# Optimization experiments

Measured on AMD Instinct MI355X. Metric: run time of the kernel, lower is better.

Reference implementation:

```python
import jax, jax.numpy as jnp
import numpy as np

C_Z = 128
C_H = 128
EPS = 1e-5


def _layer_norm(x, g, b):
    mu = jnp.mean(x, axis=-1, keepdims=True)
    var = jnp.var(x, axis=-1, keepdims=True)
    return (x - mu) * jax.lax.rsqrt(var + EPS) * g + b


def setup_inputs() -> dict:
    key = jax.random.key(0)
    ks = jax.random.split(key, 8)
    B, N = 1, 512
    z = jax.random.normal(ks[0], (B, N, N, C_Z), dtype=jnp.float32)
    mask = jnp.ones((B, N, N), dtype=jnp.float32)
    s = 0.02
    return {
        "z": z,
        "mask": mask,
        "ln_in_g": jnp.ones((C_Z,), jnp.float32),
        "ln_in_b": jnp.zeros((C_Z,), jnp.float32),
        "w_ap": jax.random.normal(ks[1], (C_Z, C_H), jnp.float32) * s,
        "b_ap": jnp.zeros((C_H,), jnp.float32),
        "w_ag": jax.random.normal(ks[2], (C_Z, C_H), jnp.float32) * s,
        "b_ag": jnp.zeros((C_H,), jnp.float32),
        "w_bp": jax.random.normal(ks[3], (C_Z, C_H), jnp.float32) * s,
        "b_bp": jnp.zeros((C_H,), jnp.float32),
        "w_bg": jax.random.normal(ks[4], (C_Z, C_H), jnp.float32) * s,
        "b_bg": jnp.zeros((C_H,), jnp.float32),
        "w_g": jax.random.normal(ks[5], (C_Z, C_Z), jnp.float32) * s,
        "b_g": jnp.zeros((C_Z,), jnp.float32),
        "ln_out_g": jnp.ones((C_H,), jnp.float32),
        "ln_out_b": jnp.zeros((C_H,), jnp.float32),
        "w_z": jax.random.normal(ks[6], (C_H, C_Z), jnp.float32) * s,
        "b_z": jnp.zeros((C_Z,), jnp.float32),
    }


def reference(z, mask, ln_in_g, ln_in_b, w_ap, b_ap, w_ag, b_ag,
              w_bp, b_bp, w_bg, b_bg, w_g, b_g, ln_out_g, ln_out_b, w_z, b_z):
    m = mask[..., None]                                  # [B,N,N,1]
    zn = _layer_norm(z, ln_in_g, ln_in_b)                # [B,N,N,Cz]
    a = m * jax.nn.sigmoid(zn @ w_ag + b_ag) * (zn @ w_ap + b_ap)  # [B,N,N,H]
    b = m * jax.nn.sigmoid(zn @ w_bg + b_bg) * (zn @ w_bp + b_bp)  # [B,N,N,H]
    # outgoing triangle: x[i,k] = sum_j a[i,j] * b[k,j]  (per hidden channel)
    x = jnp.einsum("bijh,bkjh->bikh", a, b)
    x = _layer_norm(x, ln_out_g, ln_out_b) @ w_z + b_z   # [B,N,N,Cz]
    g = jax.nn.sigmoid(zn @ w_g + b_g)
    return x * g
```

## Files before the change

### kernel.cpp

```cpp
#include <hip/hip_runtime.h>
#include <stdint.h>

#define NPOS 262144
#define EPS_LN 1e-5f
#define ZSTRIDE 272

typedef _Float16 f16x8_t __attribute__((ext_vector_type(8)));
typedef float f32x4_t __attribute__((ext_vector_type(4)));

static __device__ __forceinline__ unsigned short f2h(float f) {
    union { _Float16 h; unsigned short u; } v;
    v.h = (_Float16)f;
    return v.u;
}
static __device__ __forceinline__ float h2f(unsigned short u) {
    union { unsigned short u; _Float16 h; } v;
    v.u = u;
    return (float)v.h;
}
static __device__ __forceinline__ float sigmoidf_(float x) {
    return 1.0f / (1.0f + __expf(-x));
}

#define GLOAD_LDS16(gp, lp) __builtin_amdgcn_global_load_lds( \
    (const __attribute__((address_space(1))) void*)(gp), \
    (__attribute__((address_space(3))) void*)(lp), 16, 0, 0)

__global__ __launch_bounds__(256)
void k_prep6(const float* w0, const float* w1, const float* w2,
             const float* w3, const float* w4, const float* w5,
             const float* lng, const float* lnog, unsigned short* wt) {
    const float* srcs[6] = {w0, w1, w2, w3, w4, w5};
    const float* src = srcs[blockIdx.x];
    const float* fold = (blockIdx.x == 4) ? lnog : lng;
    unsigned short* dst = wt + blockIdx.x * 16384;
    for (int rep = 0; rep < 64; ++rep) {
        int idx = rep * 256 + threadIdx.x;
        int h = idx >> 7, k = idx & 127;
        dst[idx] = f2h(src[k * 128 + h] * fold[k]);
    }
}

__global__ __launch_bounds__(128)
void k_const(const float* wap, const float* wag, const float* wbp,
             const float* wbg, const float* wz, const float* wg,
             const float* lng, const float* lnb,
             const float* lnog, const float* lnob, float* cc) {
    const float* Ws[6] = {wap, wag, wbp, wbg, wz, wg};
    const float* W = Ws[blockIdx.x];
    const float* gv = (blockIdx.x == 4) ? lnog : lng;
    const float* bv = (blockIdx.x == 4) ? lnob : lnb;
    int c = threadIdx.x;
    float s1 = 0.f, s2 = 0.f;
    for (int k = 0; k < 128; ++k) {
        float wv = W[k * 128 + c];
        s1 += gv[k] * wv;
        s2 += bv[k] * wv;
    }
    cc[blockIdx.x * 256 + c] = s1;
    cc[blockIdx.x * 256 + 128 + c] = s2;
}

__global__ __launch_bounds__(512, 2)
void k1e(const float* __restrict__ z, const float* __restrict__ mask,
         const unsigned short* __restrict__ wt, const float* __restrict__ cc,
         const float* __restrict__ b_ap, const float* __restrict__ b_ag,
         const float* __restrict__ b_bp, const float* __restrict__ b_bg,
         unsigned short* __restrict__ a_t, unsigned short* __restrict__ b_t,
         unsigned short* __restrict__ z16, unsigned* __restrict__ mustd)
{
    __shared__ char sZ[128 * ZSTRIDE];
    __shared__ float smu[128];
    __shared__ float srstd[128];
    const int t = threadIdx.x;
    const int lane = t & 63;
    const int w = t >> 6;
    const int g = lane >> 4;
    const int l15 = lane & 15;
    const int h = w * 16 + l15;
    const int p0 = blockIdx.x * 128;

    {
        const int pos = t >> 2, q = t & 3;
        const float* zp = z + (size_t)(p0 + pos) * 128 + q * 32;
        float s = 0.f, s2 = 0.f;
        #pragma unroll
        for (int e = 0; e < 8; ++e) {
            float4 v = *(const float4*)(zp + e * 4);
            s += v.x + v.y + v.z + v.w;
            s2 += v.x * v.x + v.y * v.y + v.z * v.z + v.w * v.w;
            uint2 st;
            st.x = f2h(v.x) | ((unsigned)f2h(v.y) << 16);
            st.y = f2h(v.z) | ((unsigned)f2h(v.w) << 16);
            *(uint2*)(sZ + pos * ZSTRIDE + (q * 32 + e * 4) * 2) = st;
            *(uint2*)(z16 + (size_t)(p0 + pos) * 128 + q * 32 + e * 4) = st;
        }
        s  += __shfl_xor(s, 1);  s  += __shfl_xor(s, 2);
        s2 += __shfl_xor(s2, 1); s2 += __shfl_xor(s2, 2);
        float mu = s * (1.0f / 128.0f);
        float var = s2 * (1.0f / 128.0f) - mu * mu;
        float rstd = rsqrtf(var + EPS_LN);
        if (q == 0) {
            smu[pos] = mu;
            srstd[pos] = rstd;
            mustd[p0 + pos] = f2h(mu) | ((unsigned)f2h(rstd) << 16);
        }
    }

    f16x8_t wapf[4], wagf[4], wbpf[4], wbgf[4];
    #pragma unroll
    for (int kk = 0; kk < 4; ++kk) {
        int off = h * 128 + kk * 32 + g * 8;
        wapf[kk] = *(const f16x8_t*)(wt + 0 * 16384 + off);
        wagf[kk] = *(const f16x8_t*)(wt + 1 * 16384 + off);
        wbpf[kk] = *(const f16x8_t*)(wt + 2 * 16384 + off);
        wbgf[kk] = *(const f16x8_t*)(wt + 3 * 16384 + off);
    }
    const float C1ap = cc[0 * 256 + h], C2ap = cc[0 * 256 + 128 + h];
    const float C1ag = cc[1 * 256 + h], C2ag = cc[1 * 256 + 128 + h];
    const float C1bp = cc[2 * 256 + h], C2bp = cc[2 * 256 + 128 + h];
    const float C1bg = cc[3 * 256 + h], C2bg = cc[3 * 256 + 128 + h];
    const float bap = b_ap[h], bag = b_ag[h];
    const float bbp = b_bp[h], bbg = b_bg[h];
    __syncthreads();

    f32x4_t zero = {0.f, 0.f, 0.f, 0.f};
    for (int rt = 0; rt < 8; ++rt) {
        f32x4_t accAP = zero, accAG = zero, accBP = zero, accBG = zero;
        #pragma unroll
        for (int kk = 0; kk < 4; ++kk) {
            f16x8_t ax = *(const f16x8_t*)(sZ + (rt * 16 + l15) * ZSTRIDE + kk * 64 + g * 16);
            accAP = __builtin_amdgcn_mfma_f32_16x16x32_f16(ax, wapf[kk], accAP, 0, 0, 0);
            accAG = __builtin_amdgcn_mfma_f32_16x16x32_f16(ax, wagf[kk], accAG, 0, 0, 0);
            accBP = __builtin_amdgcn_mfma_f32_16x16x32_f16(ax, wbpf[kk], accBP, 0, 0, 0);
            accBG = __builtin_amdgcn_mfma_f32_16x16x32_f16(ax, wbgf[kk], accBG, 0, 0, 0);
        }
        int pb = p0 + rt * 16 + g * 4;
        unsigned short pka[4], pkb[4];
        #pragma unroll
        for (int r = 0; r < 4; ++r) {
            float mu = smu[rt * 16 + g * 4 + r];
            float rstd = srstd[rt * 16 + g * 4 + r];
            float vAP = rstd * (accAP[r] - mu * C1ap) + C2ap + bap;
            float vAG = rstd * (accAG[r] - mu * C1ag) + C2ag + bag;
            float vBP = rstd * (accBP[r] - mu * C1bp) + C2bp + bbp;
            float vBG = rstd * (accBG[r] - mu * C1bg) + C2bg + bbg;
            float m = mask[pb + r];
            pka[r] = f2h(m * sigmoidf_(vAG) * vAP);
            pkb[r] = f2h(m * sigmoidf_(vBG) * vBP);
        }
        uint2 sta, stb;
        sta.x = pka[0] | ((unsigned)pka[1] << 16);
        sta.y = pka[2] | ((unsigned)pka[3] << 16);
        stb.x = pkb[0] | ((unsigned)pkb[1] << 16);
        stb.y = pkb[2] | ((unsigned)pkb[3] << 16);
        *(uint2*)(a_t + (size_t)h * NPOS + pb) = sta;
        *(uint2*)(b_t + (size_t)h * NPOS + pb) = stb;
    }
}

__global__ __launch_bounds__(256, 2)
void k2_tri(const unsigned short* __restrict__ a_t,
            const unsigned short* __restrict__ b_t,
            unsigned short* __restrict__ x_t) {
    __shared__ char sA[16384];
    __shared__ char sB[16384];
    const int t = threadIdx.x;
    const int lane = t & 63;
    const int w = t >> 6;
    const int wr = w >> 1, wc = w & 1;
    const int h = blockIdx.y;
    const int i0 = (blockIdx.x >> 2) * 128;
    const int k0 = (blockIdx.x & 3) * 128;
    const unsigned short* Abase = a_t + (size_t)h * NPOS;
    const unsigned short* Bbase = b_t + (size_t)h * NPOS;

    f32x4_t zero = {0.f, 0.f, 0.f, 0.f};
    f32x4_t acc[4][4];
    #pragma unroll
    for (int m = 0; m < 4; ++m)
        #pragma unroll
        for (int n = 0; n < 4; ++n) acc[m][n] = zero;

    for (int kt = 0; kt < 8; ++kt) {
        #pragma unroll
        for (int pass = 0; pass < 4; ++pass) {
            int ci = pass * 256 + t;
            int row = ci >> 3, ch = ci & 7;
            const unsigned short* gA = Abase + (size_t)(i0 + row) * 512 + kt * 64 + ch * 8;
            const unsigned short* gB = Bbase + (size_t)(k0 + row) * 512 + kt * 64 + ch * 8;
            GLOAD_LDS16(gA, sA + w * 1024 + pass * 4096);
            GLOAD_LDS16(gB, sB + w * 1024 + pass * 4096);
        }
        __syncthreads();
        #pragma unroll
        for (int ks = 0; ks < 2; ++ks) {
            f16x8_t af[4], bf[4];
            #pragma unroll
            for (int m = 0; m < 4; ++m) {
                int ar = wr * 64 + m * 16 + (lane & 15);
                af[m] = *(const f16x8_t*)(sA + ar * 128 + ks * 64 + (lane >> 4) * 16);
            }
            #pragma unroll
            for (int n = 0; n < 4; ++n) {
                int br = wc * 64 + n * 16 + (lane & 15);
                bf[n] = *(const f16x8_t*)(sB + br * 128 + ks * 64 + (lane >> 4) * 16);
            }
            #pragma unroll
            for (int m = 0; m < 4; ++m)
                #pragma unroll
                for (int n = 0; n < 4; ++n)
                    acc[m][n] = __builtin_amdgcn_mfma_f32_16x16x32_f16(af[m], bf[n], acc[m][n], 0, 0, 0);
        }
        __syncthreads();
    }
    #pragma unroll
    for (int m = 0; m < 4; ++m) {
        int i = i0 + wr * 64 + m * 16 + (lane >> 4) * 4;
        #pragma unroll
        for (int n = 0; n < 4; ++n) {
            int k = k0 + wc * 64 + n * 16 + (lane & 15);
            #pragma unroll
            for (int r = 0; r < 4; ++r) {
                x_t[(size_t)h * NPOS + (size_t)(i + r) * 512 + k] = f2h(acc[m][n][r]);
            }
        }
    }
}

__global__ __launch_bounds__(512, 2)
void k3d(const unsigned short* __restrict__ x_t,
         const unsigned short* __restrict__ z16,
         const unsigned* __restrict__ mustd,
         const unsigned short* __restrict__ wt, const float* __restrict__ cc,
         const float* __restrict__ b_z, const float* __restrict__ b_g,
         float* __restrict__ out)
{
    __shared__ char sX[128 * ZSTRIDE];
    __shared__ float smuX[128], srstdX[128];
    __shared__ float smuZ[128], srstdZ[128];
    const int t = threadIdx.x, lane = t & 63, w = t >> 6;
    const int g = lane >> 4;
    const int c = w * 16 + (lane & 15);
    const int p0 = blockIdx.x * 128;

    f16x8_t wzf[4], wgf[4];
    #pragma unroll
    for (int kk = 0; kk < 4; ++kk) {
        int off = c * 128 + kk * 32 + g * 8;
        wzf[kk] = *(const f16x8_t*)(wt + 4 * 16384 + off);
        wgf[kk] = *(const f16x8_t*)(wt + 5 * 16384 + off);
    }
    const float bzv = b_z[c], bgv = b_g[c];
    const float C1z = cc[4 * 256 + c], C2z = cc[4 * 256 + 128 + c];
    const float C1g = cc[5 * 256 + c], C2g = cc[5 * 256 + 128 + c];

    if (t < 128) {
        unsigned v = mustd[p0 + t];
        smuZ[t] = h2f((unsigned short)(v & 0xffffu));
        srstdZ[t] = h2f((unsigned short)(v >> 16));
    }

    {
        const int hp = lane;
        const int ps = w * 16;
        const unsigned short* x0 = x_t + (size_t)(2 * hp) * NPOS + p0 + ps;
        const unsigned short* x1 = x_t + (size_t)(2 * hp + 1) * NPOS + p0 + ps;
        uint4 a0 = *(const uint4*)(x0);
        uint4 a1 = *(const uint4*)(x0 + 8);
        uint4 b0 = *(const uint4*)(x1);
        uint4 b1 = *(const uint4*)(x1 + 8);
        unsigned aw[8] = {a0.x, a0.y, a0.z, a0.w, a1.x, a1.y, a1.z, a1.w};
        unsigned bw[8] = {b0.x, b0.y, b0.z, b0.w, b1.x, b1.y, b1.z, b1.w};
        #pragma unroll
        for (int e = 0; e < 8; ++e) {
            int p = ps + 2 * e;
            *(unsigned*)(sX + p * ZSTRIDE + hp * 4) =
                (aw[e] & 0xffffu) | ((bw[e] & 0xffffu) << 16);
            *(unsigned*)(sX + (p + 1) * ZSTRIDE + hp * 4) =
                (aw[e] >> 16) | ((bw[e] >> 16) << 16);
        }
    }
    __syncthreads();
    {
        int pos = t >> 2, q = t & 3;
        float s = 0.f, s2 = 0.f;
        #pragma unroll
        for (int e = 0; e < 8; ++e) {
            uint2 vv = *(const uint2*)(sX + pos * ZSTRIDE + (q * 32 + e * 4) * 2);
            float v0 = h2f((unsigned short)(vv.x & 0xffffu));
            float v1 = h2f((unsigned short)(vv.x >> 16));
            float v2 = h2f((unsigned short)(vv.y & 0xffffu));
            float v3 = h2f((unsigned short)(vv.y >> 16));
            s  += v0 + v1 + v2 + v3;
            s2 += v0 * v0 + v1 * v1 + v2 * v2 + v3 * v3;
        }
        s  += __shfl_xor(s, 1);  s  += __shfl_xor(s, 2);
        s2 += __shfl_xor(s2, 1); s2 += __shfl_xor(s2, 2);
        float mu = s * (1.0f / 128.0f);
        float var = s2 * (1.0f / 128.0f) - mu * mu;
        if (q == 0) {
            smuX[pos] = mu;
            srstdX[pos] = rsqrtf(var + EPS_LN);
        }
    }
    __syncthreads();
    f32x4_t zero = {0.f, 0.f, 0.f, 0.f};
    for (int rt = 0; rt < 8; ++rt) {
        f32x4_t accX = zero, accG = zero;
        #pragma unroll
        for (int kk = 0; kk < 4; ++kk) {
            int row = rt * 16 + (lane & 15);
            f16x8_t ax = *(const f16x8_t*)(sX + row * ZSTRIDE + kk * 64 + g * 16);
            f16x8_t az = *(const f16x8_t*)(z16 + (size_t)(p0 + row) * 128 + kk * 32 + g * 8);
            accX = __builtin_amdgcn_mfma_f32_16x16x32_f16(ax, wzf[kk], accX, 0, 0, 0);
            accG = __builtin_amdgcn_mfma_f32_16x16x32_f16(az, wgf[kk], accG, 0, 0, 0);
        }
        int lr0 = rt * 16 + g * 4;
        #pragma unroll
        for (int r = 0; r < 4; ++r) {
            int lr = lr0 + r;
            float oz = srstdX[lr] * (accX[r] - smuX[lr] * C1z) + C2z + bzv;
            float lg = srstdZ[lr] * (accG[r] - smuZ[lr] * C1g) + C2g + bgv;
            out[(size_t)(p0 + lr) * 128 + c] = oz * sigmoidf_(lg);
        }
    }
}

extern "C" void kernel_launch(void* const* d_in, const int* in_sizes, int n_in,
                              void* d_out, int out_size, void* d_ws, size_t ws_size,
                              hipStream_t stream) {
    const float* z        = (const float*)d_in[0];
    const float* mask     = (const float*)d_in[1];
    const float* ln_in_g  = (const float*)d_in[2];
    const float* ln_in_b  = (const float*)d_in[3];
    const float* w_ap     = (const float*)d_in[4];
    const float* b_ap     = (const float*)d_in[5];
    const float* w_ag     = (const float*)d_in[6];
    const float* b_ag     = (const float*)d_in[7];
    const float* w_bp     = (const float*)d_in[8];
    const float* b_bp     = (const float*)d_in[9];
    const float* w_bg     = (const float*)d_in[10];
    const float* b_bg     = (const float*)d_in[11];
    const float* w_g      = (const float*)d_in[12];
    const float* b_g      = (const float*)d_in[13];
    const float* ln_out_g = (const float*)d_in[14];
    const float* ln_out_b = (const float*)d_in[15];
    const float* w_z      = (const float*)d_in[16];
    const float* b_z      = (const float*)d_in[17];
    float* out = (float*)d_out;

    char* ws = (char*)d_ws;
    const size_t MB64 = (size_t)NPOS * 128 * 2;
    unsigned short* wt   = (unsigned short*)(ws);
    float*          cc   = (float*)(ws + 786432);
    unsigned*      mustd = (unsigned*)(ws + (1 << 20));
    unsigned short* a_t  = (unsigned short*)(ws + (2 << 20));
    unsigned short* b_t  = (unsigned short*)(ws + (2 << 20) + MB64);
    unsigned short* x_t  = (unsigned short*)(ws + (2 << 20) + 2 * MB64);
    unsigned short* z16  = (unsigned short*)(ws + (2 << 20) + 3 * MB64);

    k_prep6<<<6, 256, 0, stream>>>(w_ap, w_ag, w_bp, w_bg, w_z, w_g,
                                   ln_in_g, ln_out_g, wt);
    k_const<<<6, 128, 0, stream>>>(w_ap, w_ag, w_bp, w_bg, w_z, w_g,
                                   ln_in_g, ln_in_b, ln_out_g, ln_out_b, cc);
    k1e<<<2048, 512, 0, stream>>>(z, mask, wt, cc,
                                  b_ap, b_ag, b_bp, b_bg,
                                  a_t, b_t, z16, mustd);
    k2_tri<<<dim3(16, 128), 256, 0, stream>>>(a_t, b_t, x_t);
    k3d<<<2048, 512, 0, stream>>>(x_t, z16, mustd, wt, cc, b_z, b_g, out);
}
```

Before: 340.6 us.

## Split z conversion and LN stats out of projection kernel into separate pass

Moves the fp32-to-fp16 conversion of z and the per-row LayerNorm statistics into a new standalone kernel. The projection kernel now reads fp16 z and the packed fp16 mu/rstd straight from global memory, with no LDS staging and no block barrier. This is meant to remove the LDS footprint and the sync from the MFMA kernel so it can run at higher occupancy. In exchange there is an extra launch, z16 is re-read from global (half the bytes of the fp32 input), and mu/rstd are now taken from fp16-rounded values, which adds a little error.

```diff
diff --git a/kernel.cpp b/kernel.cpp
--- a/kernel.cpp
+++ b/kernel.cpp
@@ -61,17 +61,41 @@
     cc[blockIdx.x * 256 + 128 + c] = s2;
 }
 
+__global__ __launch_bounds__(256)
+void k_zcvt(const float* __restrict__ z, unsigned short* __restrict__ z16,
+            unsigned* __restrict__ mustd) {
+    const int t = threadIdx.x;
+    const int row = blockIdx.x * 64 + (t >> 2);
+    const int q = t & 3;
+    const float* zp = z + (size_t)row * 128 + q * 32;
+    float s = 0.f, s2 = 0.f;
+    #pragma unroll
+    for (int e = 0; e < 8; ++e) {
+        float4 v = *(const float4*)(zp + e * 4);
+        s += v.x + v.y + v.z + v.w;
+        s2 += v.x * v.x + v.y * v.y + v.z * v.z + v.w * v.w;
+        uint2 st;
+        st.x = f2h(v.x) | ((unsigned)f2h(v.y) << 16);
+        st.y = f2h(v.z) | ((unsigned)f2h(v.w) << 16);
+        *(uint2*)(z16 + (size_t)row * 128 + q * 32 + e * 4) = st;
+    }
+    s  += __shfl_xor(s, 1);  s  += __shfl_xor(s, 2);
+    s2 += __shfl_xor(s2, 1); s2 += __shfl_xor(s2, 2);
+    float mu = s * (1.0f / 128.0f);
+    float var = s2 * (1.0f / 128.0f) - mu * mu;
+    float rstd = rsqrtf(var + EPS_LN);
+    if (q == 0) mustd[row] = f2h(mu) | ((unsigned)f2h(rstd) << 16);
+}
+
 __global__ __launch_bounds__(512, 2)
-void k1e(const float* __restrict__ z, const float* __restrict__ mask,
+void k1f(const unsigned short* __restrict__ z16,
+         const unsigned* __restrict__ mustd,
+         const float* __restrict__ mask,
          const unsigned short* __restrict__ wt, const float* __restrict__ cc,
          const float* __restrict__ b_ap, const float* __restrict__ b_ag,
          const float* __restrict__ b_bp, const float* __restrict__ b_bg,
-         unsigned short* __restrict__ a_t, unsigned short* __restrict__ b_t,
-         unsigned short* __restrict__ z16, unsigned* __restrict__ mustd)
+         unsigned short* __restrict__ a_t, unsigned short* __restrict__ b_t)
 {
-    __shared__ char sZ[128 * ZSTRIDE];
-    __shared__ float smu[128];
-    __shared__ float srstd[128];
     const int t = threadIdx.x;
     const int lane = t & 63;
     const int w = t >> 6;
@@ -80,33 +104,6 @@
     const int h = w * 16 + l15;
     const int p0 = blockIdx.x * 128;
 
-    {
-        const int pos = t >> 2, q = t & 3;
-        const float* zp = z + (size_t)(p0 + pos) * 128 + q * 32;
-        float s = 0.f, s2 = 0.f;
-        #pragma unroll
-        for (int e = 0; e < 8; ++e) {
-            float4 v = *(const float4*)(zp + e * 4);
-            s += v.x + v.y + v.z + v.w;
-            s2 += v.x * v.x + v.y * v.y + v.z * v.z + v.w * v.w;
-            uint2 st;
-            st.x = f2h(v.x) | ((unsigned)f2h(v.y) << 16);
-            st.y = f2h(v.z) | ((unsigned)f2h(v.w) << 16);
-            *(uint2*)(sZ + pos * ZSTRIDE + (q * 32 + e * 4) * 2) = st;
-            *(uint2*)(z16 + (size_t)(p0 + pos) * 128 + q * 32 + e * 4) = st;
-        }
-        s  += __shfl_xor(s, 1);  s  += __shfl_xor(s, 2);
-        s2 += __shfl_xor(s2, 1); s2 += __shfl_xor(s2, 2);
-        float mu = s * (1.0f / 128.0f);
-        float var = s2 * (1.0f / 128.0f) - mu * mu;
-        float rstd = rsqrtf(var + EPS_LN);
-        if (q == 0) {
-            smu[pos] = mu;
-            srstd[pos] = rstd;
-            mustd[p0 + pos] = f2h(mu) | ((unsigned)f2h(rstd) << 16);
-        }
-    }
-
     f16x8_t wapf[4], wagf[4], wbpf[4], wbgf[4];
     #pragma unroll
     for (int kk = 0; kk < 4; ++kk) {
@@ -122,14 +119,15 @@
     const float C1bg = cc[3 * 256 + h], C2bg = cc[3 * 256 + 128 + h];
     const float bap = b_ap[h], bag = b_ag[h];
     const float bbp = b_bp[h], bbg = b_bg[h];
-    __syncthreads();
 
     f32x4_t zero = {0.f, 0.f, 0.f, 0.f};
+    #pragma unroll 1
     for (int rt = 0; rt < 8; ++rt) {
+        const int row = p0 + rt * 16 + l15;
         f32x4_t accAP = zero, accAG = zero, accBP = zero, accBG = zero;
         #pragma unroll
         for (int kk = 0; kk < 4; ++kk) {
-            f16x8_t ax = *(const f16x8_t*)(sZ + (rt * 16 + l15) * ZSTRIDE + kk * 64 + g * 16);
+            f16x8_t ax = *(const f16x8_t*)(z16 + (size_t)row * 128 + kk * 32 + g * 8);
             accAP = __builtin_amdgcn_mfma_f32_16x16x32_f16(ax, wapf[kk], accAP, 0, 0, 0);
             accAG = __builtin_amdgcn_mfma_f32_16x16x32_f16(ax, wagf[kk], accAG, 0, 0, 0);
             accBP = __builtin_amdgcn_mfma_f32_16x16x32_f16(ax, wbpf[kk], accBP, 0, 0, 0);
@@ -139,8 +137,9 @@
         unsigned short pka[4], pkb[4];
         #pragma unroll
         for (int r = 0; r < 4; ++r) {
-            float mu = smu[rt * 16 + g * 4 + r];
-            float rstd = srstd[rt * 16 + g * 4 + r];
+            unsigned msv = mustd[pb + r];
+            float mu = h2f((unsigned short)(msv & 0xffffu));
+            float rstd = h2f((unsigned short)(msv >> 16));
             float vAP = rstd * (accAP[r] - mu * C1ap) + C2ap + bap;
             float vAG = rstd * (accAG[r] - mu * C1ag) + C2ag + bag;
             float vBP = rstd * (accBP[r] - mu * C1bp) + C2bp + bbp;
@@ -364,9 +363,9 @@
                                    ln_in_g, ln_out_g, wt);
     k_const<<<6, 128, 0, stream>>>(w_ap, w_ag, w_bp, w_bg, w_z, w_g,
                                    ln_in_g, ln_in_b, ln_out_g, ln_out_b, cc);
-    k1e<<<2048, 512, 0, stream>>>(z, mask, wt, cc,
-                                  b_ap, b_ag, b_bp, b_bg,
-                                  a_t, b_t, z16, mustd);
+    k_zcvt<<<4096, 256, 0, stream>>>(z, z16, mustd);
+    k1f<<<2048, 512, 0, stream>>>(z16, mustd, mask, wt, cc,
+                                  b_ap, b_ag, b_bp, b_bg, a_t, b_t);
     k2_tri<<<dim3(16, 128), 256, 0, stream>>>(a_t, b_t, x_t);
     k3d<<<2048, 512, 0, stream>>>(x_t, z16, mustd, wt, cc, b_z, b_g, out);
 }
```

New measurement: 371.5 us. 9.1% more time.
